# Optimization experiments

Measured on AMD Instinct MI355X. Metric: run time of the kernel, lower is better.

The kernel has to match this reference:

```python
import jax, jax.numpy as jnp
import numpy as np

ELEM_ID = 3.0  # mocked pw element id for 'agentLemming'
B, C, H, W = 16, 20, 512, 512


def _step(world, fall_left):
    # torch.roll semantics: get_above = roll(+1, H-axis), get_below = roll(-1, H-axis),
    # get_left = roll(+1, W-axis), get_right = roll(-1, W-axis)
    shift_w = 1 if fall_left else -1
    density = world[:, 1:2]                                   # [B,1,H,W]
    is_element = world[:, 0:1] == ELEM_ID                     # pw.get_bool(world,'agentLemming')
    density_forward = jnp.roll(density, shift_w, axis=3)
    density_above = jnp.roll(density, 1, axis=2)
    density_forward_above = jnp.roll(density_above, shift_w, axis=3)
    does_become_above = (is_element
                         & (density_forward - density >= 0)
                         & (density_above - density < 0)
                         & (density_forward_above - density < 0))
    does_become_below = jnp.roll(does_become_above, -1, axis=2)
    world_above = jnp.roll(world, 1, axis=2)
    world_below = jnp.roll(world, -1, axis=2)
    a = does_become_above.astype(world.dtype)                 # broadcasts [B,1,H,W] over C
    b = does_become_below.astype(world.dtype)
    # interp2: (~a & ~b)*if_false + a*if_a + b*if_b  (sums if both switches fire, as in torch)
    return (1.0 - a) * (1.0 - b) * world + a * world_above + b * world_below


def setup_inputs() -> dict:
    key = jax.random.key(0)
    k1, k2, k3, k4, k5 = jax.random.split(key, 5)
    world = jax.random.normal(k1, (B, C, H, W), dtype=jnp.float32)
    # channel 0 holds integer element ids; id 3 == agentLemming
    elem_ids = jax.random.randint(k5, (B, 1, H, W), 0, 10).astype(jnp.float32)
    world = world.at[:, 0:1].set(elem_ids)
    rand_movement = jax.random.uniform(k2, (B, 1, H, W), dtype=jnp.float32)
    rand_interact = jax.random.uniform(k3, (B, 1, H, W), dtype=jnp.float32)
    rand_element = jax.random.uniform(k4, (B, 1, H, W), dtype=jnp.float32)
    return {"world": world, "rand_movement": rand_movement,
            "rand_interact": rand_interact, "rand_element": rand_element}


def reference(world, rand_movement, rand_interact, rand_element):
    # rand_* are unpacked from info but unused by BehaviorLemming
    world = _step(world, fall_left=True)
    world = _step(world, fall_left=False)
    return world
```

## Files before the change

### kernel.cpp

```cpp
#include <hip/hip_runtime.h>

#define Bn 16
#define Cn 20
#define Hn 512
#define Wn 512
#define HWn (Hn*Wn)

__device__ unsigned char g_a1[(size_t)Bn*HWn];
__device__ unsigned char g_a2[(size_t)Bn*HWn];

__global__ __launch_bounds__(256) void mask1_kernel(const float* __restrict__ world) {
    int idx = blockIdx.x * 256 + threadIdx.x;
    int w = idx & (Wn - 1);
    int h = (idx >> 9) & (Hn - 1);
    int b = idx >> 18;
    const float* e = world + (size_t)b * Cn * HWn;
    const float* d = e + HWn;
    int wm = (w - 1) & (Wn - 1);
    int hm = (h - 1) & (Hn - 1);
    float dc  = d[h  * Wn + w];
    float df  = d[h  * Wn + wm];
    float da  = d[hm * Wn + w];
    float dfa = d[hm * Wn + wm];
    bool a = (e[h * Wn + w] == 3.0f) & (df - dc >= 0.0f) & (da - dc < 0.0f) & (dfa - dc < 0.0f);
    g_a1[idx] = (unsigned char)a;
}

__device__ __forceinline__ float stepval(const float* __restrict__ p,
                                         const unsigned char* __restrict__ a1p,
                                         int r, int wc) {
    int rm = (r - 1) & (Hn - 1), rp = (r + 1) & (Hn - 1);
    unsigned char a  = a1p[r  * Wn + wc];
    unsigned char bb = a1p[rp * Wn + wc];
    float v;
    if (a)       { v = p[rm * Wn + wc]; if (bb) v += p[rp * Wn + wc]; }
    else if (bb) { v = p[rp * Wn + wc]; }
    else         { v = p[r  * Wn + wc]; }
    return v;
}

__global__ __launch_bounds__(256) void mask2_kernel(const float* __restrict__ world) {
    int idx = blockIdx.x * 256 + threadIdx.x;
    int w = idx & (Wn - 1);
    int h = (idx >> 9) & (Hn - 1);
    int b = idx >> 18;
    const float* e = world + (size_t)b * Cn * HWn;
    const float* d = e + HWn;
    const unsigned char* a1p = g_a1 + (size_t)b * HWn;
    int wp = (w + 1) & (Wn - 1);
    int hm = (h - 1) & (Hn - 1);
    float I0   = stepval(e, a1p, h,  w);
    float I1c  = stepval(d, a1p, h,  w);
    float I1f  = stepval(d, a1p, h,  wp);
    float I1a  = stepval(d, a1p, hm, w);
    float I1fa = stepval(d, a1p, hm, wp);
    bool a = (I0 == 3.0f) & (I1f - I1c >= 0.0f) & (I1a - I1c < 0.0f) & (I1fa - I1c < 0.0f);
    g_a2[idx] = (unsigned char)a;
}

__global__ __launch_bounds__(256) void final_kernel(const float* __restrict__ world,
                                                    float* __restrict__ out) {
    int idx = blockIdx.x * 256 + threadIdx.x;
    int wq = idx & (Wn / 4 - 1);
    int h  = (idx >> 7) & (Hn - 1);
    int b  = idx >> 16;
    int w  = wq * 4;

    const unsigned char* a1p = g_a1 + (size_t)b * HWn;
    const unsigned char* a2p = g_a2 + (size_t)b * HWn;
    int hm2 = (h - 2) & (Hn - 1), hm1 = (h - 1) & (Hn - 1);
    int hp1 = (h + 1) & (Hn - 1), hp2 = (h + 2) & (Hn - 1);

    float cm2[4], cm1[4], c0[4], cp1[4], cp2[4];
#pragma unroll
    for (int j = 0; j < 4; j++) {
        int wc = w + j;
        float r_m1 = (float)a1p[hm1 * Wn + wc];
        float r_0  = (float)a1p[h   * Wn + wc];
        float r_p1 = (float)a1p[hp1 * Wn + wc];
        float r_p2 = (float)a1p[hp2 * Wn + wc];
        float s0 = (float)a2p[h   * Wn + wc];
        float s1 = (float)a2p[hp1 * Wn + wc];
        float A2m = s0, A2p = s1, A2z = (1.f - s0) * (1.f - s1);
        cm2[j] = A2m * r_m1;
        cm1[j] = A2m * (1.f - r_m1) * (1.f - r_0) + A2z * r_0;
        c0[j]  = A2m * r_0 + A2z * (1.f - r_0) * (1.f - r_p1) + A2p * r_p1;
        cp1[j] = A2z * r_p1 + A2p * (1.f - r_p1) * (1.f - r_p2);
        cp2[j] = A2p * r_p2;
    }

    const float* base  = world + (size_t)b * Cn * HWn;
    float*       obase = out   + (size_t)b * Cn * HWn;
#pragma unroll 4
    for (int c = 0; c < Cn; c++) {
        const float* p = base + (size_t)c * HWn;
        float4 x_m2 = *(const float4*)(p + hm2 * Wn + w);
        float4 x_m1 = *(const float4*)(p + hm1 * Wn + w);
        float4 x_0  = *(const float4*)(p + h   * Wn + w);
        float4 x_p1 = *(const float4*)(p + hp1 * Wn + w);
        float4 x_p2 = *(const float4*)(p + hp2 * Wn + w);
        float4 r;
        r.x = cm2[0]*x_m2.x + cm1[0]*x_m1.x + c0[0]*x_0.x + cp1[0]*x_p1.x + cp2[0]*x_p2.x;
        r.y = cm2[1]*x_m2.y + cm1[1]*x_m1.y + c0[1]*x_0.y + cp1[1]*x_p1.y + cp2[1]*x_p2.y;
        r.z = cm2[2]*x_m2.z + cm1[2]*x_m1.z + c0[2]*x_0.z + cp1[2]*x_p1.z + cp2[2]*x_p2.z;
        r.w = cm2[3]*x_m2.w + cm1[3]*x_m1.w + c0[3]*x_0.w + cp1[3]*x_p1.w + cp2[3]*x_p2.w;
        *(float4*)(obase + (size_t)c * HWn + h * Wn + w) = r;
    }
}

extern "C" void kernel_launch(void* const* d_in, const int* in_sizes, int n_in,
                              void* d_out, int out_size, void* d_ws, size_t ws_size,
                              hipStream_t stream) {
    const float* world = (const float*)d_in[0];
    float* out = (float*)d_out;

    mask1_kernel<<<(Bn * HWn) / 256, 256, 0, stream>>>(world);
    mask2_kernel<<<(Bn * HWn) / 256, 256, 0, stream>>>(world);
    final_kernel<<<(Bn * Hn * (Wn / 4)) / 256, 256, 0, stream>>>(world, out);
}
```

Measured before the change: 691.3 us.

## Fuse mask and stencil kernels into one row-tiled kernel with shared-memory masks

Replaces the three kernels with one fused kernel. Each block handles a 16-row band of one batch and half the channels, computes both step masks for the band plus halo into shared memory, and packs the five stencil coefficients per pixel into a 16-bit code. It then applies the 5-tap vertical stencil over register-cached rows and writes with nontemporal stores. This removes the global mask round trips and two launches, and it reuses loaded rows across eight output rows. The cost is that mask work is recomputed for the halo rows and in both channel-half blocks, and the block index is swizzled to spread work.

Measured after the change: 761.6 us. 1.1x slower.

```diff
diff --git a/kernel.cpp b/kernel.cpp
--- a/kernel.cpp
+++ b/kernel.cpp
@@ -5,106 +5,145 @@
 #define Hn 512
 #define Wn 512
 #define HWn (Hn*Wn)
+#define Rr 16
+#define NA1 (Rr+3)
+#define NA2 (Rr+1)
 
-__device__ unsigned char g_a1[(size_t)Bn*HWn];
-__device__ unsigned char g_a2[(size_t)Bn*HWn];
+typedef float nfloat4 __attribute__((ext_vector_type(4)));
 
-__global__ __launch_bounds__(256) void mask1_kernel(const float* __restrict__ world) {
-    int idx = blockIdx.x * 256 + threadIdx.x;
-    int w = idx & (Wn - 1);
-    int h = (idx >> 9) & (Hn - 1);
-    int b = idx >> 18;
-    const float* e = world + (size_t)b * Cn * HWn;
-    const float* d = e + HWn;
-    int wm = (w - 1) & (Wn - 1);
-    int hm = (h - 1) & (Hn - 1);
-    float dc  = d[h  * Wn + w];
-    float df  = d[h  * Wn + wm];
-    float da  = d[hm * Wn + w];
-    float dfa = d[hm * Wn + wm];
-    bool a = (e[h * Wn + w] == 3.0f) & (df - dc >= 0.0f) & (da - dc < 0.0f) & (dfa - dc < 0.0f);
-    g_a1[idx] = (unsigned char)a;
+__device__ __forceinline__ float sv(float pm, float pc, float pp, int a, int bb) {
+    float t  = bb ? pp : 0.0f;
+    float v1 = pm + t;
+    float v2 = bb ? pp : pc;
+    return a ? v1 : v2;
 }
 
-__device__ __forceinline__ float stepval(const float* __restrict__ p,
-                                         const unsigned char* __restrict__ a1p,
-                                         int r, int wc) {
-    int rm = (r - 1) & (Hn - 1), rp = (r + 1) & (Hn - 1);
-    unsigned char a  = a1p[r  * Wn + wc];
-    unsigned char bb = a1p[rp * Wn + wc];
-    float v;
-    if (a)       { v = p[rm * Wn + wc]; if (bb) v += p[rp * Wn + wc]; }
-    else if (bb) { v = p[rp * Wn + wc]; }
-    else         { v = p[r  * Wn + wc]; }
-    return v;
-}
+__global__ __launch_bounds__(256, 4) void fused_kernel(const float* __restrict__ world,
+                                                       float* __restrict__ out) {
+    __shared__ unsigned char  sa1[NA1][Wn];
+    __shared__ unsigned char  sa2[NA2][Wn];
+    __shared__ unsigned short sco[Rr][Wn];
 
-__global__ __launch_bounds__(256) void mask2_kernel(const float* __restrict__ world) {
-    int idx = blockIdx.x * 256 + threadIdx.x;
-    int w = idx & (Wn - 1);
-    int h = (idx >> 9) & (Hn - 1);
-    int b = idx >> 18;
-    const float* e = world + (size_t)b * Cn * HWn;
-    const float* d = e + HWn;
-    const unsigned char* a1p = g_a1 + (size_t)b * HWn;
-    int wp = (w + 1) & (Wn - 1);
-    int hm = (h - 1) & (Hn - 1);
-    float I0   = stepval(e, a1p, h,  w);
-    float I1c  = stepval(d, a1p, h,  w);
-    float I1f  = stepval(d, a1p, h,  wp);
-    float I1a  = stepval(d, a1p, hm, w);
-    float I1fa = stepval(d, a1p, hm, wp);
-    bool a = (I0 == 3.0f) & (I1f - I1c >= 0.0f) & (I1a - I1c < 0.0f) & (I1fa - I1c < 0.0f);
-    g_a2[idx] = (unsigned char)a;
-}
+    int bid = blockIdx.x;
+    int v   = (bid >> 3) | ((bid & 7) << 7);
+    int chalf = v & 1;
+    int hg    = (v >> 1) & 31;
+    int b     = v >> 6;
+    int h0    = hg * Rr;
+    int tid   = threadIdx.x;
 
-__global__ __launch_bounds__(256) void final_kernel(const float* __restrict__ world,
-                                                    float* __restrict__ out) {
-    int idx = blockIdx.x * 256 + threadIdx.x;
-    int wq = idx & (Wn / 4 - 1);
-    int h  = (idx >> 7) & (Hn - 1);
-    int b  = idx >> 16;
+    const float* base = world + (size_t)b * Cn * HWn;
+    const float* e = base;
+    const float* d = base + HWn;
+
+    for (int col = 0; col < 2; ++col) {
+        int w  = tid + col * 256;
+        int wm = (w - 1) & (Wn - 1);
+        int r0 = (h0 - 2) & (Hn - 1);
+        float dmw = d[r0 * Wn + w];
+        float dmm = d[r0 * Wn + wm];
+#pragma unroll
+        for (int i = 0; i < NA1; ++i) {
+            int r = (h0 - 1 + i) & (Hn - 1);
+            float dc = d[r * Wn + w];
+            float df = d[r * Wn + wm];
+            float ec = e[r * Wn + w];
+            bool a = (ec == 3.0f) & (df - dc >= 0.0f) & (dmw - dc < 0.0f) & (dmm - dc < 0.0f);
+            sa1[i][w] = (unsigned char)a;
+            dmw = dc; dmm = df;
+        }
+    }
+    __syncthreads();
+
+    for (int col = 0; col < 2; ++col) {
+        int w  = tid + col * 256;
+        int wp = (w + 1) & (Wn - 1);
+        float dwa = d[((h0 - 2) & (Hn - 1)) * Wn + w];
+        float dwb = d[((h0 - 1) & (Hn - 1)) * Wn + w];
+        float dwc = d[h0 * Wn + w];
+        float dwd = d[((h0 + 1) & (Hn - 1)) * Wn + w];
+        float dpa = d[((h0 - 2) & (Hn - 1)) * Wn + wp];
+        float dpb = d[((h0 - 1) & (Hn - 1)) * Wn + wp];
+        float dpc = d[h0 * Wn + wp];
+        float dpd = d[((h0 + 1) & (Hn - 1)) * Wn + wp];
+        float ewa = e[((h0 - 1) & (Hn - 1)) * Wn + w];
+        float ewb = e[h0 * Wn + w];
+        float ewc = e[((h0 + 1) & (Hn - 1)) * Wn + w];
+#pragma unroll
+        for (int i2 = 0; i2 < NA2; ++i2) {
+            int a_hm = sa1[i2][w],  a_h = sa1[i2 + 1][w],  a_hp = sa1[i2 + 2][w];
+            int b_hm = sa1[i2][wp], b_h = sa1[i2 + 1][wp], b_hp = sa1[i2 + 2][wp];
+            float I0   = sv(ewa, ewb, ewc, a_h, a_hp);
+            float I1c  = sv(dwb, dwc, dwd, a_h, a_hp);
+            float I1f  = sv(dpb, dpc, dpd, b_h, b_hp);
+            float I1a  = sv(dwa, dwb, dwc, a_hm, a_h);
+            float I1fa = sv(dpa, dpb, dpc, b_hm, b_h);
+            bool av = (I0 == 3.0f) & (I1f - I1c >= 0.0f) & (I1a - I1c < 0.0f) & (I1fa - I1c < 0.0f);
+            sa2[i2][w] = (unsigned char)av;
+            int rn = (h0 + i2 + 2) & (Hn - 1);
+            dwa = dwb; dwb = dwc; dwc = dwd; dwd = d[rn * Wn + w];
+            dpa = dpb; dpb = dpc; dpc = dpd; dpd = d[rn * Wn + wp];
+            ewa = ewb; ewb = ewc; ewc = e[rn * Wn + w];
+        }
+    }
+    __syncthreads();
+
+#pragma unroll
+    for (int k = 0; k < 32; ++k) {
+        int idx = k * 256 + tid;
+        int j2 = idx >> 9;
+        int w  = idx & (Wn - 1);
+        int rm1 = sa1[j2][w], r0v = sa1[j2 + 1][w], rp1 = sa1[j2 + 2][w], rp2 = sa1[j2 + 3][w];
+        int s0 = sa2[j2][w], s1 = sa2[j2 + 1][w];
+        int z  = (1 - s0) * (1 - s1);
+        int cm2 = s0 * rm1;
+        int cm1 = s0 * (1 - rm1) * (1 - r0v) + z * r0v;
+        int c0  = s0 * r0v + z * (1 - r0v) * (1 - rp1) + s1 * rp1;
+        int cp1 = z * rp1 + s1 * (1 - rp1) * (1 - rp2);
+        int cp2 = s1 * rp2;
+        sco[j2][w] = (unsigned short)(cm2 | (cm1 << 2) | (c0 << 4) | (cp1 << 6) | (cp2 << 8));
+    }
+    __syncthreads();
+
+    int wq = tid & 127;
+    int rh = tid >> 7;
     int w  = wq * 4;
+    int j0 = rh * 8;
+    float* obase = out + (size_t)b * Cn * HWn;
+    int cstart = chalf * 10;
 
-    const unsigned char* a1p = g_a1 + (size_t)b * HWn;
-    const unsigned char* a2p = g_a2 + (size_t)b * HWn;
-    int hm2 = (h - 2) & (Hn - 1), hm1 = (h - 1) & (Hn - 1);
-    int hp1 = (h + 1) & (Hn - 1), hp2 = (h + 2) & (Hn - 1);
-
-    float cm2[4], cm1[4], c0[4], cp1[4], cp2[4];
+    for (int c = cstart; c < cstart + 10; ++c) {
+        const float* p = base + (size_t)c * HWn;
+        nfloat4 x[12];
 #pragma unroll
-    for (int j = 0; j < 4; j++) {
-        int wc = w + j;
-        float r_m1 = (float)a1p[hm1 * Wn + wc];
-        float r_0  = (float)a1p[h   * Wn + wc];
-        float r_p1 = (float)a1p[hp1 * Wn + wc];
-        float r_p2 = (float)a1p[hp2 * Wn + wc];
-        float s0 = (float)a2p[h   * Wn + wc];
-        float s1 = (float)a2p[hp1 * Wn + wc];
-        float A2m = s0, A2p = s1, A2z = (1.f - s0) * (1.f - s1);
-        cm2[j] = A2m * r_m1;
-        cm1[j] = A2m * (1.f - r_m1) * (1.f - r_0) + A2z * r_0;
-        c0[j]  = A2m * r_0 + A2z * (1.f - r_0) * (1.f - r_p1) + A2p * r_p1;
-        cp1[j] = A2z * r_p1 + A2p * (1.f - r_p1) * (1.f - r_p2);
-        cp2[j] = A2p * r_p2;
-    }
-
-    const float* base  = world + (size_t)b * Cn * HWn;
-    float*       obase = out   + (size_t)b * Cn * HWn;
-#pragma unroll 4
-    for (int c = 0; c < Cn; c++) {
-        const float* p = base + (size_t)c * HWn;
-        float4 x_m2 = *(const float4*)(p + hm2 * Wn + w);
-        float4 x_m1 = *(const float4*)(p + hm1 * Wn + w);
-        float4 x_0  = *(const float4*)(p + h   * Wn + w);
-        float4 x_p1 = *(const float4*)(p + hp1 * Wn + w);
-        float4 x_p2 = *(const float4*)(p + hp2 * Wn + w);
-        float4 r;
-        r.x = cm2[0]*x_m2.x + cm1[0]*x_m1.x + c0[0]*x_0.x + cp1[0]*x_p1.x + cp2[0]*x_p2.x;
-        r.y = cm2[1]*x_m2.y + cm1[1]*x_m1.y + c0[1]*x_0.y + cp1[1]*x_p1.y + cp2[1]*x_p2.y;
-        r.z = cm2[2]*x_m2.z + cm1[2]*x_m1.z + c0[2]*x_0.z + cp1[2]*x_p1.z + cp2[2]*x_p2.z;
-        r.w = cm2[3]*x_m2.w + cm1[3]*x_m1.w + c0[3]*x_0.w + cp1[3]*x_p1.w + cp2[3]*x_p2.w;
-        *(float4*)(obase + (size_t)c * HWn + h * Wn + w) = r;
+        for (int i = 0; i < 12; ++i) {
+            int r = (h0 + j0 - 2 + i) & (Hn - 1);
+            x[i] = *(const nfloat4*)(p + r * Wn + w);
+        }
+        float* op = obase + (size_t)c * HWn + (size_t)(h0 + j0) * Wn + w;
+#pragma unroll
+        for (int j = 0; j < 8; ++j) {
+            int j2 = j0 + j;
+            uint2 q = *(const uint2*)&sco[j2][w];
+            unsigned qa = q.x & 0xffffu;
+            unsigned qb = q.x >> 16;
+            unsigned qc = q.y & 0xffffu;
+            unsigned qd = q.y >> 16;
+            nfloat4 r4;
+            r4.x = (float)(qa & 3) * x[j].x + (float)((qa >> 2) & 3) * x[j + 1].x
+                 + (float)((qa >> 4) & 3) * x[j + 2].x + (float)((qa >> 6) & 3) * x[j + 3].x
+                 + (float)((qa >> 8) & 3) * x[j + 4].x;
+            r4.y = (float)(qb & 3) * x[j].y + (float)((qb >> 2) & 3) * x[j + 1].y
+                 + (float)((qb >> 4) & 3) * x[j + 2].y + (float)((qb >> 6) & 3) * x[j + 3].y
+                 + (float)((qb >> 8) & 3) * x[j + 4].y;
+            r4.z = (float)(qc & 3) * x[j].z + (float)((qc >> 2) & 3) * x[j + 1].z
+                 + (float)((qc >> 4) & 3) * x[j + 2].z + (float)((qc >> 6) & 3) * x[j + 3].z
+                 + (float)((qc >> 8) & 3) * x[j + 4].z;
+            r4.w = (float)(qd & 3) * x[j].w + (float)((qd >> 2) & 3) * x[j + 1].w
+                 + (float)((qd >> 4) & 3) * x[j + 2].w + (float)((qd >> 6) & 3) * x[j + 3].w
+                 + (float)((qd >> 8) & 3) * x[j + 4].w;
+            __builtin_nontemporal_store(r4, (nfloat4*)(op + j * Wn));
+        }
     }
 }
 
@@ -113,8 +152,5 @@
                               hipStream_t stream) {
     const float* world = (const float*)d_in[0];
     float* out = (float*)d_out;
-
-    mask1_kernel<<<(Bn * HWn) / 256, 256, 0, stream>>>(world);
-    mask2_kernel<<<(Bn * HWn) / 256, 256, 0, stream>>>(world);
-    final_kernel<<<(Bn * Hn * (Wn / 4)) / 256, 256, 0, stream>>>(world, out);
+    fused_kernel<<<Bn * (Hn / Rr) * 2, 256, 0, stream>>>(world, out);
 }
```
